# Kernel tuning notes

Measured on AMD Instinct MI355X. Metric: run time of the kernel, lower is better.

The kernel has to match this reference:

```python
import jax, jax.numpy as jnp
import numpy as np

EMBED_DIM = 512
NUM_HEADS = 8
HEAD_DIM = EMBED_DIM // NUM_HEADS


def setup_inputs() -> dict:
    key = jax.random.key(0)
    ks = jax.random.split(key, 9)
    s = 1.0 / np.sqrt(EMBED_DIM)
    x = jax.random.normal(ks[0], (2, 4096, EMBED_DIM), dtype=jnp.float32)
    return {
        "x": x,
        "Wq": jax.random.uniform(ks[1], (EMBED_DIM, EMBED_DIM), jnp.float32, -s, s),
        "bq": jax.random.uniform(ks[2], (EMBED_DIM,), jnp.float32, -s, s),
        "Wk": jax.random.uniform(ks[3], (EMBED_DIM, EMBED_DIM), jnp.float32, -s, s),
        "bk": jax.random.uniform(ks[4], (EMBED_DIM,), jnp.float32, -s, s),
        "Wv": jax.random.uniform(ks[5], (EMBED_DIM, EMBED_DIM), jnp.float32, -s, s),
        "bv": jax.random.uniform(ks[6], (EMBED_DIM,), jnp.float32, -s, s),
        "Wo": jax.random.uniform(ks[7], (EMBED_DIM, EMBED_DIM), jnp.float32, -s, s),
        "bo": jax.random.uniform(ks[8], (EMBED_DIM,), jnp.float32, -s, s),
    }


def reference(x, Wq, bq, Wk, bk, Wv, bv, Wo, bo):
    B, S, E = x.shape
    H, D = NUM_HEADS, HEAD_DIM
    # projections (torch Linear: x @ W.T + b)
    q = (x @ Wq.T + bq).reshape(B, S, H, D).transpose(0, 2, 1, 3)  # [B,H,S,D]
    k = (x @ Wk.T + bk).reshape(B, S, H, D).transpose(0, 2, 1, 3)
    v = (x @ Wv.T + bv).reshape(B, S, H, D).transpose(0, 2, 1, 3)
    scores = jnp.einsum("bhsd,bhtd->bhst", q, k) / np.sqrt(D)  # [B,H,S,S]
    attn = jax.nn.softmax(scores, axis=-1)
    out = jnp.einsum("bhst,bhtd->bhsd", attn, v)  # [B,H,S,D]
    out = out.transpose(0, 2, 1, 3).reshape(B, S, E)
    return out @ Wo.T + bo + x
```

## Files before the change

kernel.cpp:

```cpp
#include <hip/hip_runtime.h>
#include <hip/hip_bf16.h>


typedef __attribute__((ext_vector_type(8))) short short8;
typedef __attribute__((ext_vector_type(4))) short short4v;
typedef __attribute__((ext_vector_type(4))) float floatx4;
typedef __attribute__((ext_vector_type(2))) float floatx2;

#define SEQ 4096
#define EMB 512
#define NH 8
#define HD 64
#define MROWS 8192
#define SC2 0.18033688011112042f

__device__ inline unsigned short f2bf_rne(float f) {
    union { float f; unsigned int u; } c; c.f = f;
    unsigned int u = c.u;
    return (unsigned short)((u + 0x7FFFu + ((u >> 16) & 1u)) >> 16);
}

__device__ inline short8 load8f(const float* __restrict__ p) {
    float4 a = *(const float4*)p;
    float4 b = *(const float4*)(p + 4);
    short8 r;
    r[0] = (short)f2bf_rne(a.x); r[1] = (short)f2bf_rne(a.y);
    r[2] = (short)f2bf_rne(a.z); r[3] = (short)f2bf_rne(a.w);
    r[4] = (short)f2bf_rne(b.x); r[5] = (short)f2bf_rne(b.y);
    r[6] = (short)f2bf_rne(b.z); r[7] = (short)f2bf_rne(b.w);
    return r;
}

__device__ inline void gload_lds16(const unsigned short* g, unsigned short* l) {
    __builtin_amdgcn_global_load_lds(
        (__attribute__((address_space(1))) void*)(void*)g,
        (__attribute__((address_space(3))) void*)l,
        16, 0, 0);
}

__device__ inline unsigned int pk_bf2(float a, float b) {
    union { float f; unsigned int u; } ca, cb; ca.f = a; cb.f = b;
    return __builtin_amdgcn_perm(cb.u + 0x8000u, ca.u + 0x8000u, 0x07060302u);
}

__global__ __launch_bounds__(256) void convert_kernel(
    const float* __restrict__ x, const float* __restrict__ Wq,
    const float* __restrict__ Wk, const float* __restrict__ Wv,
    const float* __restrict__ Wo, unsigned short* __restrict__ xb,
    unsigned short* __restrict__ wb)
{
    const size_t i8 = ((size_t)blockIdx.x * 256 + threadIdx.x) * 8;
    const float* src; unsigned short* dst;
    if (i8 < (size_t)MROWS * EMB) { src = x + i8; dst = xb + i8; }
    else {
        size_t j = i8 - (size_t)MROWS * EMB;
        int w = (int)(j >> 18); size_t off = j & 262143;
        src = (w == 0 ? Wq : w == 1 ? Wk : w == 2 ? Wv : Wo) + off;
        dst = wb + (size_t)w * 262144 + off;
    }
    *(short8*)dst = load8f(src);
}

__global__ __launch_bounds__(256) void qkv_kernel(
    const unsigned short* __restrict__ xb, const unsigned short* __restrict__ wb,
    const float* __restrict__ bq, const float* __restrict__ bk,
    const float* __restrict__ bv, unsigned short* __restrict__ Qo,
    unsigned short* __restrict__ Ko, unsigned short* __restrict__ VTo)
{
    __shared__ unsigned short smem[32768];

    const int tid = threadIdx.x, wave = tid >> 6, lane = tid & 63;
    const int quad = lane >> 4, l16 = lane & 15;
    const int wm = wave >> 1, wn = wave & 1;
    const int row0 = blockIdx.x * 128, col0 = blockIdx.y * 128;
    const int z = blockIdx.z;

    unsigned short* sA = smem;
    unsigned short* sB = smem + 16384;

    const unsigned short* A = xb + (size_t)row0 * EMB;
    const unsigned short* Bm = wb + (size_t)z * 262144 + (size_t)col0 * EMB;
    const float* bias = z == 0 ? bq : z == 1 ? bk : bv;
    unsigned short* out = z == 0 ? Qo : z == 1 ? Ko : VTo;

    auto stage = [&](int buf, int k0) {
#pragma unroll
        for (int it = 0; it < 4; ++it) {
            const int s = it * 256 + tid;
            const int row = s >> 3, cg = (s & 7) ^ (row & 7);
            const size_t go = (size_t)row * EMB + k0 + cg * 8;
            gload_lds16(A + go, &sA[buf * 8192 + (it * 256 + wave * 64) * 8]);
            gload_lds16(Bm + go, &sB[buf * 8192 + (it * 256 + wave * 64) * 8]);
        }
    };

    floatx4 acc[4][4];
#pragma unroll
    for (int i = 0; i < 4; ++i)
#pragma unroll
        for (int j = 0; j < 4; ++j) { floatx4 zz = {0.f,0.f,0.f,0.f}; acc[i][j] = zz; }

    stage(0, 0);
    int buf = 0;
    for (int k0 = 0; k0 < EMB; k0 += 64) {
        __syncthreads();
        if (k0 + 64 < EMB) stage(buf ^ 1, k0 + 64);
#pragma unroll
        for (int kk = 0; kk < 2; ++kk) {
            short8 a[4], b[4];
#pragma unroll
            for (int mi = 0; mi < 4; ++mi)
                a[mi] = *(const short8*)&sA[buf * 8192 + (wm * 64 + mi * 16 + l16) * 64 + (((kk * 4 + quad) ^ (l16 & 7)) << 3)];
#pragma unroll
            for (int ni = 0; ni < 4; ++ni)
                b[ni] = *(const short8*)&sB[buf * 8192 + (wn * 64 + ni * 16 + l16) * 64 + (((kk * 4 + quad) ^ (l16 & 7)) << 3)];
            if (z != 2) {
#pragma unroll
                for (int i = 0; i < 4; ++i)
#pragma unroll
                    for (int j = 0; j < 4; ++j)
                        acc[i][j] = __builtin_amdgcn_mfma_f32_16x16x32_bf16(b[i], a[j], acc[i][j], 0, 0, 0);
            } else {
#pragma unroll
                for (int i = 0; i < 4; ++i)
#pragma unroll
                    for (int j = 0; j < 4; ++j)
                        acc[i][j] = __builtin_amdgcn_mfma_f32_16x16x32_bf16(a[i], b[j], acc[i][j], 0, 0, 0);
            }
        }
        buf ^= 1;
    }

    __syncthreads();
    unsigned short* ct = smem;
    const float qs = (z == 0) ? SC2 : 1.0f;
    if (z != 2) {
#pragma unroll
        for (int i = 0; i < 4; ++i) {
            const int n0 = wn * 64 + i * 16 + quad * 4;
            const float4 fb = *(const float4*)&bias[col0 + n0];
#pragma unroll
            for (int j = 0; j < 4; ++j) {
                const int m = wm * 64 + j * 16 + l16;
                ushort4 pk;
                pk.x = f2bf_rne((acc[i][j][0] + fb.x) * qs);
                pk.y = f2bf_rne((acc[i][j][1] + fb.y) * qs);
                pk.z = f2bf_rne((acc[i][j][2] + fb.z) * qs);
                pk.w = f2bf_rne((acc[i][j][3] + fb.w) * qs);
                *(ushort4*)&ct[m * 132 + n0] = pk;
            }
        }
    } else {
#pragma unroll
        for (int j = 0; j < 4; ++j) {
            const int n = wn * 64 + j * 16 + l16;
            const float fb = bias[col0 + n];
#pragma unroll
            for (int i = 0; i < 4; ++i) {
                const int m0 = wm * 64 + i * 16 + quad * 4;
                ushort4 pk;
                pk.x = f2bf_rne(acc[i][j][0] + fb);
                pk.y = f2bf_rne(acc[i][j][1] + fb);
                pk.z = f2bf_rne(acc[i][j][2] + fb);
                pk.w = f2bf_rne(acc[i][j][3] + fb);
                *(ushort4*)&ct[n * 132 + m0] = pk;
            }
        }
    }
    __syncthreads();
#pragma unroll
    for (int it = 0; it < 8; ++it) {
        const int idx = it * 256 + tid;
        const int row = idx >> 4, chunk = idx & 15;
        short8 v = *(const short8*)&ct[row * 132 + chunk * 8];
        size_t addr;
        if (z != 2) {
            const int m_g = row0 + row;
            const int b = m_g >> 12, s = m_g & 4095;
            const int n_g = col0 + chunk * 8;
            const int h = n_g >> 6, d = n_g & 63;
            addr = ((size_t)((b * NH + h) * SEQ + s)) * HD + d;
        } else {
            const int n_g = col0 + row;
            const int h = n_g >> 6, d = n_g & 63;
            const int m_g = row0 + chunk * 8;
            const int b = m_g >> 12, s0 = m_g & 4095;
            addr = ((size_t)((b * NH + h) * HD + d)) * SEQ + s0;
        }
        *(short8*)&out[addr] = v;
    }
}

__global__ __launch_bounds__(256) void attn_kernel(
    const unsigned short* __restrict__ Q, const unsigned short* __restrict__ K,
    const unsigned short* __restrict__ VT, unsigned short* __restrict__ Oout)
{
    __shared__ unsigned short sK[2][4096];
    __shared__ unsigned short sVT[2][4096];

    const int tid = threadIdx.x, wave = tid >> 6, lane = tid & 63;
    const int quad = lane >> 4, l16 = lane & 15;
    const int bh = blockIdx.x, q0 = blockIdx.y * 128;

    const unsigned short* Qh = Q + (size_t)bh * SEQ * HD;
    const unsigned short* Kh = K + (size_t)bh * SEQ * HD;
    const unsigned short* Vh = VT + (size_t)bh * HD * SEQ;

    short8 qf[2][2];
#pragma unroll
    for (int mi = 0; mi < 2; ++mi)
#pragma unroll
        for (int kk = 0; kk < 2; ++kk)
            qf[mi][kk] = *(const short8*)(Qh + (size_t)(q0 + wave * 32 + mi * 16 + l16) * HD + kk * 32 + quad * 8);

    floatx4 oacc[2][4];
#pragma unroll
    for (int mi = 0; mi < 2; ++mi)
#pragma unroll
        for (int dt = 0; dt < 4; ++dt) { floatx4 zz = {0.f,0.f,0.f,0.f}; oacc[mi][dt] = zz; }
    floatx2 psum2[2] = {{0.f, 0.f}, {0.f, 0.f}};

    auto stage = [&](int buf, int t0) {
#pragma unroll
        for (int psi = 0; psi < 2; ++psi) {
            const int r = psi * 32 + wave * 8 + (lane >> 3);
            const int c = (lane & 7) ^ (r & 7);
            gload_lds16(Kh + (size_t)(t0 + r) * HD + c * 8, &sK[buf][psi * 2048 + wave * 512]);
            gload_lds16(Vh + (size_t)r * SEQ + t0 + c * 8, &sVT[buf][psi * 2048 + wave * 512]);
        }
    };

    stage(0, 0);
    int buf = 0;
    for (int t0 = 0; t0 < SEQ; t0 += 64) {
        __syncthreads();
        if (t0 + 64 < SEQ) stage(buf ^ 1, t0 + 64);

        floatx4 stf[2][4];
#pragma unroll
        for (int mi = 0; mi < 2; ++mi)
#pragma unroll
            for (int nt = 0; nt < 4; ++nt) { floatx4 zz = {0.f,0.f,0.f,0.f}; stf[mi][nt] = zz; }
#pragma unroll
        for (int kk = 0; kk < 2; ++kk) {
            short8 bK[4];
#pragma unroll
            for (int nt = 0; nt < 4; ++nt)
                bK[nt] = *(const short8*)&sK[buf][(nt * 16 + l16) * 64 + (((kk * 4 + quad) ^ (l16 & 7)) << 3)];
#pragma unroll
            for (int mi = 0; mi < 2; ++mi)
#pragma unroll
                for (int nt = 0; nt < 4; ++nt)
                    stf[mi][nt] = __builtin_amdgcn_mfma_f32_16x16x32_bf16(bK[nt], qf[mi][kk], stf[mi][nt], 0, 0, 0);
        }

        short4v paf[2][4];
#pragma unroll
        for (int mi = 0; mi < 2; ++mi)
#pragma unroll
            for (int nt = 0; nt < 4; ++nt) {
                const float p0 = __builtin_amdgcn_exp2f(stf[mi][nt][0]);
                const float p1 = __builtin_amdgcn_exp2f(stf[mi][nt][1]);
                const float p2 = __builtin_amdgcn_exp2f(stf[mi][nt][2]);
                const float p3 = __builtin_amdgcn_exp2f(stf[mi][nt][3]);
                floatx2 a = {p0, p1}, b = {p2, p3};
                psum2[mi] += a + b;
                union { uint2 u; short4v s; } cv;
                cv.u.x = pk_bf2(p0, p1);
                cv.u.y = pk_bf2(p2, p3);
                paf[mi][nt] = cv.s;
            }

#pragma unroll
        for (int nt = 0; nt < 4; ++nt) {
            short4v bv[4];
#pragma unroll
            for (int dt = 0; dt < 4; ++dt)
                bv[dt] = *(const short4v*)&sVT[buf][(dt * 16 + l16) * 64 +
                         (((nt * 2 + (quad >> 1)) ^ (l16 & 7)) << 3) + (quad & 1) * 4];
#pragma unroll
            for (int mi = 0; mi < 2; ++mi)
#pragma unroll
                for (int dt = 0; dt < 4; ++dt)
                    oacc[mi][dt] = __builtin_amdgcn_mfma_f32_16x16x16bf16_1k(paf[mi][nt], bv[dt], oacc[mi][dt], 0, 0, 0);
        }
        buf ^= 1;
    }

    float psum[2];
#pragma unroll
    for (int mi = 0; mi < 2; ++mi) {
        psum[mi] = psum2[mi][0] + psum2[mi][1];
        psum[mi] += __shfl_xor(psum[mi], 16);
        psum[mi] += __shfl_xor(psum[mi], 32);
    }

    const int b = bh >> 3, h = bh & 7;
#pragma unroll
    for (int mi = 0; mi < 2; ++mi)
#pragma unroll
        for (int r = 0; r < 4; ++r) {
            const float inv = 1.0f / __shfl(psum[mi], quad * 4 + r);
            const int s = q0 + wave * 32 + mi * 16 + quad * 4 + r;
            const size_t base = ((size_t)b * SEQ + s) * EMB + h * HD;
#pragma unroll
            for (int dt = 0; dt < 4; ++dt)
                Oout[base + dt * 16 + l16] = f2bf_rne(oacc[mi][dt][r] * inv);
        }
}

__global__ __launch_bounds__(256) void outproj_kernel(
    const unsigned short* __restrict__ Ain, const unsigned short* __restrict__ wob,
    const float* __restrict__ bias, const float* __restrict__ X,
    float* __restrict__ out)
{
    __shared__ unsigned short sA[2][4096];
    __shared__ unsigned short sB[2][8192];

    const int tid = threadIdx.x, wave = tid >> 6, lane = tid & 63;
    const int quad = lane >> 4, l16 = lane & 15;
    const int wm = wave >> 1, wn = wave & 1;
    const int row0 = blockIdx.x * 64, col0 = blockIdx.y * 128;

    const unsigned short* A = Ain + (size_t)row0 * EMB;
    const unsigned short* Bm = wob + (size_t)col0 * EMB;

    auto stage = [&](int buf, int k0) {
#pragma unroll
        for (int it = 0; it < 2; ++it) {
            const int s = it * 256 + tid;
            const int row = s >> 3, cg = (s & 7) ^ (row & 7);
            gload_lds16(A + (size_t)row * EMB + k0 + cg * 8, &sA[buf][(it * 256 + wave * 64) * 8]);
        }
#pragma unroll
        for (int it = 0; it < 4; ++it) {
            const int s = it * 256 + tid;
            const int row = s >> 3, cg = (s & 7) ^ (row & 7);
            gload_lds16(Bm + (size_t)row * EMB + k0 + cg * 8, &sB[buf][(it * 256 + wave * 64) * 8]);
        }
    };

    floatx4 acc[2][4];
#pragma unroll
    for (int mi = 0; mi < 2; ++mi)
#pragma unroll
        for (int ni = 0; ni < 4; ++ni) { floatx4 zz = {0.f,0.f,0.f,0.f}; acc[mi][ni] = zz; }

    stage(0, 0);
    int buf = 0;
    for (int k0 = 0; k0 < EMB; k0 += 64) {
        __syncthreads();
        if (k0 + 64 < EMB) stage(buf ^ 1, k0 + 64);
#pragma unroll
        for (int kk = 0; kk < 2; ++kk) {
            short8 a[2], b[4];
#pragma unroll
            for (int mi = 0; mi < 2; ++mi)
                a[mi] = *(const short8*)&sA[buf][(wm * 32 + mi * 16 + l16) * 64 + (((kk * 4 + quad) ^ (l16 & 7)) << 3)];
#pragma unroll
            for (int ni = 0; ni < 4; ++ni)
                b[ni] = *(const short8*)&sB[buf][(wn * 64 + ni * 16 + l16) * 64 + (((kk * 4 + quad) ^ (l16 & 7)) << 3)];
#pragma unroll
            for (int mi = 0; mi < 2; ++mi)
#pragma unroll
                for (int ni = 0; ni < 4; ++ni)
                    acc[mi][ni] = __builtin_amdgcn_mfma_f32_16x16x32_bf16(a[mi], b[ni], acc[mi][ni], 0, 0, 0);
        }
        buf ^= 1;
    }

#pragma unroll
    for (int mi = 0; mi < 2; ++mi)
#pragma unroll
        for (int ni = 0; ni < 4; ++ni) {
            const int n = col0 + wn * 64 + ni * 16 + l16;
            const float bs = bias[n];
#pragma unroll
            for (int r = 0; r < 4; ++r) {
                const int m = row0 + wm * 32 + mi * 16 + quad * 4 + r;
                const size_t idx = (size_t)m * EMB + n;
                out[idx] = acc[mi][ni][r] + bs + X[idx];
            }
        }
}

extern "C" void kernel_launch(void* const* d_in, const int* in_sizes, int n_in,
                              void* d_out, int out_size, void* d_ws, size_t ws_size,
                              hipStream_t stream) {
    const float* x  = (const float*)d_in[0];
    const float* Wq = (const float*)d_in[1];
    const float* bq = (const float*)d_in[2];
    const float* Wk = (const float*)d_in[3];
    const float* bk = (const float*)d_in[4];
    const float* Wv = (const float*)d_in[5];
    const float* bv = (const float*)d_in[6];
    const float* Wo = (const float*)d_in[7];
    const float* bo = (const float*)d_in[8];
    float* out = (float*)d_out;

    const size_t SZ = (size_t)MROWS * EMB;
    unsigned short* wsXB = (unsigned short*)d_ws;
    unsigned short* wsWB = wsXB + SZ;
    unsigned short* wsQ  = wsWB + 4 * 262144;
    unsigned short* wsK  = wsQ + SZ;
    unsigned short* wsVT = wsK + SZ;

    convert_kernel<<<2560, 256, 0, stream>>>(x, Wq, Wk, Wv, Wo, wsXB, wsWB);
    qkv_kernel<<<dim3(MROWS / 128, EMB / 128, 3), 256, 0, stream>>>(
        wsXB, wsWB, bq, bk, bv, wsQ, wsK, wsVT);
    attn_kernel<<<dim3(2 * NH, SEQ / 128), 256, 0, stream>>>(wsQ, wsK, wsVT, wsXB);
    outproj_kernel<<<dim3(MROWS / 64, EMB / 128), 256, 0, stream>>>(
        wsXB, wsWB + 3 * 262144, bo, x, out);
}
```

Before: 206.0 us.

## Fuse fp32-to-bf16 conversion into GEMM loads and switch attention to 32x32 MFMA

```diff
diff --git a/kernel.cpp b/kernel.cpp
--- a/kernel.cpp
+++ b/kernel.cpp
@@ -6,6 +6,7 @@
 typedef __attribute__((ext_vector_type(4))) short short4v;
 typedef __attribute__((ext_vector_type(4))) float floatx4;
 typedef __attribute__((ext_vector_type(2))) float floatx2;
+typedef __attribute__((ext_vector_type(16))) float floatx16;
 
 #define SEQ 4096
 #define EMB 512
@@ -20,20 +21,9 @@
     return (unsigned short)((u + 0x7FFFu + ((u >> 16) & 1u)) >> 16);
 }
 
-__device__ inline short8 load8f(const float* __restrict__ p) {
-    float4 a = *(const float4*)p;
-    float4 b = *(const float4*)(p + 4);
-    short8 r;
-    r[0] = (short)f2bf_rne(a.x); r[1] = (short)f2bf_rne(a.y);
-    r[2] = (short)f2bf_rne(a.z); r[3] = (short)f2bf_rne(a.w);
-    r[4] = (short)f2bf_rne(b.x); r[5] = (short)f2bf_rne(b.y);
-    r[6] = (short)f2bf_rne(b.z); r[7] = (short)f2bf_rne(b.w);
-    return r;
-}
-
-__device__ inline void gload_lds16(const unsigned short* g, unsigned short* l) {
+__device__ inline void gload_lds16(const void* g, void* l) {
     __builtin_amdgcn_global_load_lds(
-        (__attribute__((address_space(1))) void*)(void*)g,
+        (const __attribute__((address_space(1))) void*)g,
         (__attribute__((address_space(3))) void*)l,
         16, 0, 0);
 }
@@ -43,31 +33,25 @@
     return __builtin_amdgcn_perm(cb.u + 0x8000u, ca.u + 0x8000u, 0x07060302u);
 }
 
-__global__ __launch_bounds__(256) void convert_kernel(
-    const float* __restrict__ x, const float* __restrict__ Wq,
+__device__ inline short8 frag8f(const float* p0, const float* p1) {
+    float4 u = *(const float4*)p0;
+    float4 v = *(const float4*)p1;
+    union { uint4 u4; short8 s8; } cv;
+    cv.u4.x = pk_bf2(u.x, u.y); cv.u4.y = pk_bf2(u.z, u.w);
+    cv.u4.z = pk_bf2(v.x, v.y); cv.u4.w = pk_bf2(v.z, v.w);
+    return cv.s8;
+}
+
+__global__ __launch_bounds__(256) void qkv_kernel(
+    const float* __restrict__ X, const float* __restrict__ Wq,
     const float* __restrict__ Wk, const float* __restrict__ Wv,
-    const float* __restrict__ Wo, unsigned short* __restrict__ xb,
-    unsigned short* __restrict__ wb)
-{
-    const size_t i8 = ((size_t)blockIdx.x * 256 + threadIdx.x) * 8;
-    const float* src; unsigned short* dst;
-    if (i8 < (size_t)MROWS * EMB) { src = x + i8; dst = xb + i8; }
-    else {
-        size_t j = i8 - (size_t)MROWS * EMB;
-        int w = (int)(j >> 18); size_t off = j & 262143;
-        src = (w == 0 ? Wq : w == 1 ? Wk : w == 2 ? Wv : Wo) + off;
-        dst = wb + (size_t)w * 262144 + off;
-    }
-    *(short8*)dst = load8f(src);
-}
-
-__global__ __launch_bounds__(256) void qkv_kernel(
-    const unsigned short* __restrict__ xb, const unsigned short* __restrict__ wb,
     const float* __restrict__ bq, const float* __restrict__ bk,
     const float* __restrict__ bv, unsigned short* __restrict__ Qo,
     unsigned short* __restrict__ Ko, unsigned short* __restrict__ VTo)
 {
-    __shared__ unsigned short smem[32768];
+    __shared__ float fs[16384];
+    float* fsA = fs;
+    float* fsB = fs + 8192;
 
     const int tid = threadIdx.x, wave = tid >> 6, lane = tid & 63;
     const int quad = lane >> 4, l16 = lane & 15;
@@ -75,45 +59,45 @@
     const int row0 = blockIdx.x * 128, col0 = blockIdx.y * 128;
     const int z = blockIdx.z;
 
-    unsigned short* sA = smem;
-    unsigned short* sB = smem + 16384;
-
-    const unsigned short* A = xb + (size_t)row0 * EMB;
-    const unsigned short* Bm = wb + (size_t)z * 262144 + (size_t)col0 * EMB;
+    const float* A = X + (size_t)row0 * EMB;
+    const float* W = z == 0 ? Wq : z == 1 ? Wk : Wv;
+    const float* Bm = W + (size_t)col0 * EMB;
     const float* bias = z == 0 ? bq : z == 1 ? bk : bv;
     unsigned short* out = z == 0 ? Qo : z == 1 ? Ko : VTo;
 
-    auto stage = [&](int buf, int k0) {
-#pragma unroll
-        for (int it = 0; it < 4; ++it) {
+    floatx4 acc[4][4];
+#pragma unroll
+    for (int i = 0; i < 4; ++i)
+#pragma unroll
+        for (int j = 0; j < 4; ++j) { floatx4 zz = {0.f,0.f,0.f,0.f}; acc[i][j] = zz; }
+
+    for (int k0 = 0; k0 < EMB; k0 += 64) {
+        __syncthreads();
+#pragma unroll
+        for (int it = 0; it < 8; ++it) {
             const int s = it * 256 + tid;
-            const int row = s >> 3, cg = (s & 7) ^ (row & 7);
-            const size_t go = (size_t)row * EMB + k0 + cg * 8;
-            gload_lds16(A + go, &sA[buf * 8192 + (it * 256 + wave * 64) * 8]);
-            gload_lds16(Bm + go, &sB[buf * 8192 + (it * 256 + wave * 64) * 8]);
-        }
-    };
-
-    floatx4 acc[4][4];
-#pragma unroll
-    for (int i = 0; i < 4; ++i)
-#pragma unroll
-        for (int j = 0; j < 4; ++j) { floatx4 zz = {0.f,0.f,0.f,0.f}; acc[i][j] = zz; }
-
-    stage(0, 0);
-    int buf = 0;
-    for (int k0 = 0; k0 < EMB; k0 += 64) {
-        __syncthreads();
-        if (k0 + 64 < EMB) stage(buf ^ 1, k0 + 64);
+            const int row = s >> 4, c = (s & 15) ^ (row & 7);
+            gload_lds16(A + (size_t)row * EMB + k0 + c * 4, &fsA[(it * 256 + wave * 64) * 4]);
+            gload_lds16(Bm + (size_t)row * EMB + k0 + c * 4, &fsB[(it * 256 + wave * 64) * 4]);
+        }
+        __syncthreads();
 #pragma unroll
         for (int kk = 0; kk < 2; ++kk) {
             short8 a[4], b[4];
 #pragma unroll
-            for (int mi = 0; mi < 4; ++mi)
-                a[mi] = *(const short8*)&sA[buf * 8192 + (wm * 64 + mi * 16 + l16) * 64 + (((kk * 4 + quad) ^ (l16 & 7)) << 3)];
-#pragma unroll
-            for (int ni = 0; ni < 4; ++ni)
-                b[ni] = *(const short8*)&sB[buf * 8192 + (wn * 64 + ni * 16 + l16) * 64 + (((kk * 4 + quad) ^ (l16 & 7)) << 3)];
+            for (int mi = 0; mi < 4; ++mi) {
+                const int row = wm * 64 + mi * 16 + l16, rm = row & 7;
+                const int c0 = kk * 8 + 2 * quad;
+                a[mi] = frag8f(&fsA[row * 64 + ((c0 ^ rm) << 2)],
+                               &fsA[row * 64 + (((c0 + 1) ^ rm) << 2)]);
+            }
+#pragma unroll
+            for (int ni = 0; ni < 4; ++ni) {
+                const int row = wn * 64 + ni * 16 + l16, rm = row & 7;
+                const int c0 = kk * 8 + 2 * quad;
+                b[ni] = frag8f(&fsB[row * 64 + ((c0 ^ rm) << 2)],
+                               &fsB[row * 64 + (((c0 + 1) ^ rm) << 2)]);
+            }
             if (z != 2) {
 #pragma unroll
                 for (int i = 0; i < 4; ++i)
@@ -128,11 +112,10 @@
                         acc[i][j] = __builtin_amdgcn_mfma_f32_16x16x32_bf16(a[i], b[j], acc[i][j], 0, 0, 0);
             }
         }
-        buf ^= 1;
     }
 
     __syncthreads();
-    unsigned short* ct = smem;
+    unsigned short* ct = (unsigned short*)fs;
     const float qs = (z == 0) ? SC2 : 1.0f;
     if (z != 2) {
 #pragma unroll
@@ -199,26 +182,22 @@
     __shared__ unsigned short sVT[2][4096];
 
     const int tid = threadIdx.x, wave = tid >> 6, lane = tid & 63;
-    const int quad = lane >> 4, l16 = lane & 15;
+    const int l32 = lane & 31, hi = lane >> 5;
     const int bh = blockIdx.x, q0 = blockIdx.y * 128;
 
     const unsigned short* Qh = Q + (size_t)bh * SEQ * HD;
     const unsigned short* Kh = K + (size_t)bh * SEQ * HD;
     const unsigned short* Vh = VT + (size_t)bh * HD * SEQ;
 
-    short8 qf[2][2];
-#pragma unroll
-    for (int mi = 0; mi < 2; ++mi)
-#pragma unroll
-        for (int kk = 0; kk < 2; ++kk)
-            qf[mi][kk] = *(const short8*)(Qh + (size_t)(q0 + wave * 32 + mi * 16 + l16) * HD + kk * 32 + quad * 8);
-
-    floatx4 oacc[2][4];
-#pragma unroll
-    for (int mi = 0; mi < 2; ++mi)
-#pragma unroll
-        for (int dt = 0; dt < 4; ++dt) { floatx4 zz = {0.f,0.f,0.f,0.f}; oacc[mi][dt] = zz; }
-    floatx2 psum2[2] = {{0.f, 0.f}, {0.f, 0.f}};
+    short8 qf[4];
+#pragma unroll
+    for (int kk = 0; kk < 4; ++kk)
+        qf[kk] = *(const short8*)(Qh + (size_t)(q0 + wave * 32 + l32) * HD + kk * 16 + hi * 8);
+
+    const floatx16 z16 = {0.f,0.f,0.f,0.f,0.f,0.f,0.f,0.f,0.f,0.f,0.f,0.f,0.f,0.f,0.f,0.f};
+    floatx16 oacc[2];
+    oacc[0] = z16; oacc[1] = z16;
+    floatx2 psum2 = {0.f, 0.f};
 
     auto stage = [&](int buf, int t0) {
 #pragma unroll
@@ -236,86 +215,77 @@
         __syncthreads();
         if (t0 + 64 < SEQ) stage(buf ^ 1, t0 + 64);
 
-        floatx4 stf[2][4];
-#pragma unroll
-        for (int mi = 0; mi < 2; ++mi)
-#pragma unroll
-            for (int nt = 0; nt < 4; ++nt) { floatx4 zz = {0.f,0.f,0.f,0.f}; stf[mi][nt] = zz; }
-#pragma unroll
-        for (int kk = 0; kk < 2; ++kk) {
-            short8 bK[4];
-#pragma unroll
-            for (int nt = 0; nt < 4; ++nt)
-                bK[nt] = *(const short8*)&sK[buf][(nt * 16 + l16) * 64 + (((kk * 4 + quad) ^ (l16 & 7)) << 3)];
-#pragma unroll
-            for (int mi = 0; mi < 2; ++mi)
-#pragma unroll
-                for (int nt = 0; nt < 4; ++nt)
-                    stf[mi][nt] = __builtin_amdgcn_mfma_f32_16x16x32_bf16(bK[nt], qf[mi][kk], stf[mi][nt], 0, 0, 0);
+        floatx16 stf[2];
+#pragma unroll
+        for (int th = 0; th < 2; ++th) {
+            const int row = th * 32 + l32, rm = l32 & 7;
+            short8 aK = *(const short8*)&sK[buf][row * 64 + (((0 * 2 + hi) ^ rm) << 3)];
+            stf[th] = __builtin_amdgcn_mfma_f32_32x32x16_bf16(aK, qf[0], z16, 0, 0, 0);
+#pragma unroll
+            for (int kk = 1; kk < 4; ++kk) {
+                aK = *(const short8*)&sK[buf][row * 64 + (((kk * 2 + hi) ^ rm) << 3)];
+                stf[th] = __builtin_amdgcn_mfma_f32_32x32x16_bf16(aK, qf[kk], stf[th], 0, 0, 0);
+            }
         }
 
         short4v paf[2][4];
 #pragma unroll
-        for (int mi = 0; mi < 2; ++mi)
-#pragma unroll
-            for (int nt = 0; nt < 4; ++nt) {
-                const float p0 = __builtin_amdgcn_exp2f(stf[mi][nt][0]);
-                const float p1 = __builtin_amdgcn_exp2f(stf[mi][nt][1]);
-                const float p2 = __builtin_amdgcn_exp2f(stf[mi][nt][2]);
-                const float p3 = __builtin_amdgcn_exp2f(stf[mi][nt][3]);
-                floatx2 a = {p0, p1}, b = {p2, p3};
-                psum2[mi] += a + b;
-                union { uint2 u; short4v s; } cv;
+        for (int th = 0; th < 2; ++th)
+#pragma unroll
+            for (int s = 0; s < 4; ++s) {
+                const float p0 = __builtin_amdgcn_exp2f(stf[th][4 * s + 0]);
+                const float p1 = __builtin_amdgcn_exp2f(stf[th][4 * s + 1]);
+                const float p2 = __builtin_amdgcn_exp2f(stf[th][4 * s + 2]);
+                const float p3 = __builtin_amdgcn_exp2f(stf[th][4 * s + 3]);
+                floatx2 pa = {p0, p1}, pb = {p2, p3};
+                psum2 += pa + pb;
+                union { uint2 u; short4v s4; } cv;
                 cv.u.x = pk_bf2(p0, p1);
                 cv.u.y = pk_bf2(p2, p3);
-                paf[mi][nt] = cv.s;
-            }
-
-#pragma unroll
-        for (int nt = 0; nt < 4; ++nt) {
-            short4v bv[4];
-#pragma unroll
-            for (int dt = 0; dt < 4; ++dt)
-                bv[dt] = *(const short4v*)&sVT[buf][(dt * 16 + l16) * 64 +
-                         (((nt * 2 + (quad >> 1)) ^ (l16 & 7)) << 3) + (quad & 1) * 4];
-#pragma unroll
-            for (int mi = 0; mi < 2; ++mi)
-#pragma unroll
-                for (int dt = 0; dt < 4; ++dt)
-                    oacc[mi][dt] = __builtin_amdgcn_mfma_f32_16x16x16bf16_1k(paf[mi][nt], bv[dt], oacc[mi][dt], 0, 0, 0);
+                paf[th][s] = cv.s4;
+            }
+
+#pragma unroll
+        for (int dh = 0; dh < 2; ++dh) {
+            const int row = dh * 32 + l32, rm = l32 & 7;
+#pragma unroll
+            for (int th = 0; th < 2; ++th)
+#pragma unroll
+                for (int s = 0; s < 4; ++s) {
+                    short4v bv = *(const short4v*)&sVT[buf][row * 64 +
+                                 (((th * 4 + s) ^ rm) << 3) + hi * 4];
+                    oacc[dh] = __builtin_amdgcn_mfma_f32_32x32x8bf16_1k(paf[th][s], bv, oacc[dh], 0, 0, 0);
+                }
         }
         buf ^= 1;
     }
 
-    float psum[2];
-#pragma unroll
-    for (int mi = 0; mi < 2; ++mi) {
-        psum[mi] = psum2[mi][0] + psum2[mi][1];
-        psum[mi] += __shfl_xor(psum[mi], 16);
-        psum[mi] += __shfl_xor(psum[mi], 32);
-    }
+    float psum = psum2[0] + psum2[1];
+    psum += __shfl_xor(psum, 32);
+    const float inv = 1.0f / psum;
 
     const int b = bh >> 3, h = bh & 7;
 #pragma unroll
-    for (int mi = 0; mi < 2; ++mi)
-#pragma unroll
-        for (int r = 0; r < 4; ++r) {
-            const float inv = 1.0f / __shfl(psum[mi], quad * 4 + r);
-            const int s = q0 + wave * 32 + mi * 16 + quad * 4 + r;
-            const size_t base = ((size_t)b * SEQ + s) * EMB + h * HD;
-#pragma unroll
-            for (int dt = 0; dt < 4; ++dt)
-                Oout[base + dt * 16 + l16] = f2bf_rne(oacc[mi][dt][r] * inv);
-        }
+    for (int dh = 0; dh < 2; ++dh)
+#pragma unroll
+        for (int rr = 0; rr < 4; ++rr)
+#pragma unroll
+            for (int j = 0; j < 4; ++j) {
+                const int qrow = j + 8 * rr + 4 * hi;
+                const float v = oacc[dh][rr * 4 + j] * __shfl(inv, qrow);
+                const int s = q0 + wave * 32 + qrow;
+                const int d = dh * 32 + l32;
+                Oout[((size_t)b * SEQ + s) * EMB + h * HD + d] = f2bf_rne(v);
+            }
 }
 
 __global__ __launch_bounds__(256) void outproj_kernel(
-    const unsigned short* __restrict__ Ain, const unsigned short* __restrict__ wob,
+    const unsigned short* __restrict__ Ain, const float* __restrict__ Wo,
     const float* __restrict__ bias, const float* __restrict__ X,
     float* __restrict__ out)
 {
-    __shared__ unsigned short sA[2][4096];
-    __shared__ unsigned short sB[2][8192];
+    __shared__ unsigned short osA[4096];
+    __shared__ float ofsB[8192];
 
     const int tid = threadIdx.x, wave = tid >> 6, lane = tid & 63;
     const int quad = lane >> 4, l16 = lane & 15;
@@ -323,50 +293,50 @@
     const int row0 = blockIdx.x * 64, col0 = blockIdx.y * 128;
 
     const unsigned short* A = Ain + (size_t)row0 * EMB;
-    const unsigned short* Bm = wob + (size_t)col0 * EMB;
-
-    auto stage = [&](int buf, int k0) {
+    const float* Bm = Wo + (size_t)col0 * EMB;
+
+    floatx4 acc[2][4];
+#pragma unroll
+    for (int mi = 0; mi < 2; ++mi)
+#pragma unroll
+        for (int ni = 0; ni < 4; ++ni) { floatx4 zz = {0.f,0.f,0.f,0.f}; acc[mi][ni] = zz; }
+
+    for (int k0 = 0; k0 < EMB; k0 += 64) {
+        __syncthreads();
 #pragma unroll
         for (int it = 0; it < 2; ++it) {
             const int s = it * 256 + tid;
-            const int row = s >> 3, cg = (s & 7) ^ (row & 7);
-            gload_lds16(A + (size_t)row * EMB + k0 + cg * 8, &sA[buf][(it * 256 + wave * 64) * 8]);
-        }
-#pragma unroll
-        for (int it = 0; it < 4; ++it) {
+            const int row = s >> 3, c = (s & 7) ^ (row & 7);
+            gload_lds16(A + (size_t)row * EMB + k0 + c * 8, &osA[(it * 256 + wave * 64) * 8]);
+        }
+#pragma unroll
+        for (int it = 0; it < 8; ++it) {
             const int s = it * 256 + tid;
-            const int row = s >> 3, cg = (s & 7) ^ (row & 7);
-            gload_lds16(Bm + (size_t)row * EMB + k0 + cg * 8, &sB[buf][(it * 256 + wave * 64) * 8]);
-        }
-    };
-
-    floatx4 acc[2][4];
-#pragma unroll
-    for (int mi = 0; mi < 2; ++mi)
-#pragma unroll
-        for (int ni = 0; ni < 4; ++ni) { floatx4 zz = {0.f,0.f,0.f,0.f}; acc[mi][ni] = zz; }
-
-    stage(0, 0);
-    int buf = 0;
-    for (int k0 = 0; k0 < EMB; k0 += 64) {
-        __syncthreads();
-        if (k0 + 64 < EMB) stage(buf ^ 1, k0 + 64);
+            const int row = s >> 4, c = (s & 15) ^ (row & 7);
+            gload_lds16(Bm + (size_t)row * EMB + k0 + c * 4, &ofsB[(it * 256 + wave * 64) * 4]);
+        }
+        __syncthreads();
 #pragma unroll
         for (int kk = 0; kk < 2; ++kk) {
             short8 a[2], b[4];
 #pragma unroll
-            for (int mi = 0; mi < 2; ++mi)
-                a[mi] = *(const short8*)&sA[buf][(wm * 32 + mi * 16 + l16) * 64 + (((kk * 4 + quad) ^ (l16 & 7)) << 3)];
-#pragma unroll
-            for (int ni = 0; ni < 4; ++ni)
-                b[ni] = *(const short8*)&sB[buf][(wn * 64 + ni * 16 + l16) * 64 + (((kk * 4 + quad) ^ (l16 & 7)) << 3)];
+            for (int mi = 0; mi < 2; ++mi) {
+                const int row = wm * 32 + mi * 16 + l16;
+                a[mi] = *(const short8*)&osA[row * 64 + (((kk * 4 + quad) ^ (row & 7)) << 3)];
+            }
+#pragma unroll
+            for (int ni = 0; ni < 4; ++ni) {
+                const int row = wn * 64 + ni * 16 + l16, rm = row & 7;
+                const int c0 = kk * 8 + 2 * quad;
+                b[ni] = frag8f(&ofsB[row * 64 + ((c0 ^ rm) << 2)],
+                               &ofsB[row * 64 + (((c0 + 1) ^ rm) << 2)]);
+            }
 #pragma unroll
             for (int mi = 0; mi < 2; ++mi)
 #pragma unroll
                 for (int ni = 0; ni < 4; ++ni)
                     acc[mi][ni] = __builtin_amdgcn_mfma_f32_16x16x32_bf16(a[mi], b[ni], acc[mi][ni], 0, 0, 0);
         }
-        buf ^= 1;
     }
 
 #pragma unroll
@@ -399,16 +369,14 @@
     float* out = (float*)d_out;
 
     const size_t SZ = (size_t)MROWS * EMB;
-    unsigned short* wsXB = (unsigned short*)d_ws;
-    unsigned short* wsWB = wsXB + SZ;
-    unsigned short* wsQ  = wsWB + 4 * 262144;
+    unsigned short* wsQ  = (unsigned short*)d_ws;
     unsigned short* wsK  = wsQ + SZ;
     unsigned short* wsVT = wsK + SZ;
-
-    convert_kernel<<<2560, 256, 0, stream>>>(x, Wq, Wk, Wv, Wo, wsXB, wsWB);
+    unsigned short* wsO  = wsVT + SZ;
+
     qkv_kernel<<<dim3(MROWS / 128, EMB / 128, 3), 256, 0, stream>>>(
-        wsXB, wsWB, bq, bk, bv, wsQ, wsK, wsVT);
-    attn_kernel<<<dim3(2 * NH, SEQ / 128), 256, 0, stream>>>(wsQ, wsK, wsVT, wsXB);
+        x, Wq, Wk, Wv, bq, bk, bv, wsQ, wsK, wsVT);
+    attn_kernel<<<dim3(2 * NH, SEQ / 128), 256, 0, stream>>>(wsQ, wsK, wsVT, wsO);
     outproj_kernel<<<dim3(MROWS / 64, EMB / 128), 256, 0, stream>>>(
-        wsXB, wsWB + 3 * 262144, bo, x, out);
-}
+        wsO, Wo, bo, x, out);
+}
```

Result: slower. 236.5 us (+14.8%).
